# Kernel tuning notes

Measured on AMD Instinct MI355X. Metric: run time of the kernel, lower is better.

## Reference

```python
import jax, jax.numpy as jnp
import numpy as np

IN_EPS = 1e-3   # torch InstanceNorm2d eps in this module
BN_EPS = 1e-5   # torch BatchNorm2d default eps
KNN_K = 6


def instance_norm(x):
    # x: (B, C, N, 1); normalize per (batch, channel) over spatial dims (affine=False)
    m = jnp.mean(x, axis=(2, 3), keepdims=True)
    v = jnp.var(x, axis=(2, 3), keepdims=True)
    return (x - m) / jnp.sqrt(v + IN_EPS)


def batch_norm(x, gamma, beta):
    # training-mode BatchNorm2d: batch statistics over (B, H, W), biased var
    m = jnp.mean(x, axis=(0, 2, 3), keepdims=True)
    v = jnp.var(x, axis=(0, 2, 3), keepdims=True)
    xn = (x - m) / jnp.sqrt(v + BN_EPS)
    return xn * gamma[None, :, None, None] + beta[None, :, None, None]


def conv1x1(x, w, b):
    # x: (B, Cin, N, K), w: (Cout, Cin), b: (Cout,)
    return jnp.einsum('bcnk,oc->bonk', x, w) + b[None, :, None, None]


def graph_feature(x, k):
    # x: (B, C, P). KNN in feature space + edge feature [x_i, x_i - x_j].
    B, C, P = x.shape
    sq = jnp.sum(x * x, axis=1)                      # (B, P)
    gram = jnp.einsum('bcn,bcm->bnm', x, x)          # (B, P, P)
    pd = 2.0 * gram - sq[:, :, None] - sq[:, None, :]  # negative squared distance
    idx = jax.lax.top_k(pd, k)[1]                    # (B, P, k) nearest (incl. self)
    xt = jnp.transpose(x, (0, 2, 1))                 # (B, P, C)
    neigh = jnp.take_along_axis(xt, idx.reshape(B, P * k)[:, :, None], axis=1)
    neigh = neigh.reshape(B, P, k, C)
    center = jnp.broadcast_to(xt[:, :, None, :], (B, P, k, C))
    edge = jnp.concatenate([center, center - neigh], axis=3)  # (B, P, k, 2C)
    return jnp.transpose(edge, (0, 3, 1, 2))         # (B, 2C, P, k)


def reference(data, dp_gamma, dp_beta, dp_w, dp_b, du_gamma, du_beta, du_w, du_b,
              dg_w1, dg_b1, dg_g1, dg_bb1, dg_w2, dg_b2, dg_g2, dg_bb2, sc_w, sc_b):
    x = data                                         # (B, C=128, N, 1)
    # ---- diff_pool ----
    h = jax.nn.relu(batch_norm(instance_norm(x), dp_gamma, dp_beta))
    embed = conv1x1(h, dp_w, dp_b)                   # (B, K=256, N, 1)
    S = jax.nn.softmax(embed[..., 0], axis=2)        # softmax over points -> (B, K, N)
    x_down = jnp.einsum('bcn,bkn->bck', x[..., 0], S)  # (B, C, K)
    feats = jnp.transpose(x_down, (0, 2, 1))         # transpose(1,2): (B, K, C)
    # ---- DGCNN_MAX_Block: channels=K=256, points=C=128, k=6 ----
    edge = graph_feature(feats, KNN_K)               # (B, 2K, C, k)
    g = jax.nn.relu(batch_norm(conv1x1(edge, dg_w1, dg_b1), dg_g1, dg_bb1))
    g = jax.nn.relu(batch_norm(conv1x1(g, dg_w2, dg_b2), dg_g2, dg_bb2))
    g = jnp.max(g, axis=3)                           # max over neighbors -> (B, K, C)
    x2 = jnp.transpose(g, (0, 2, 1))                 # (B, C, K)
    # ---- diff_unpool ----
    h2 = jax.nn.relu(batch_norm(instance_norm(x), du_gamma, du_beta))
    embed2 = conv1x1(h2, du_w, du_b)                 # (B, K, N, 1)
    S2 = jax.nn.softmax(embed2[..., 0], axis=1)      # softmax over clusters -> (B, K, N)
    x_up = jnp.einsum('bck,bkn->bcn', x2, S2)[..., None]  # (B, C, N, 1)
    out = jnp.concatenate([x, x_up], axis=1)         # (B, 2C, N, 1)
    return conv1x1(out, sc_w, sc_b)                  # (B, C, N, 1)


def setup_inputs() -> dict:
    B, C, N, K = 16, 128, 8192, 256
    ks = jax.random.split(jax.random.key(0), 8)
    s = 0.05
    return {
        'data': jax.random.normal(ks[0], (B, C, N, 1), dtype=jnp.float32),
        'dp_gamma': jnp.ones((C,), jnp.float32), 'dp_beta': jnp.zeros((C,), jnp.float32),
        'dp_w': jax.random.normal(ks[1], (K, C), dtype=jnp.float32) * s,
        'dp_b': jnp.zeros((K,), jnp.float32),
        'du_gamma': jnp.ones((C,), jnp.float32), 'du_beta': jnp.zeros((C,), jnp.float32),
        'du_w': jax.random.normal(ks[2], (K, C), dtype=jnp.float32) * s,
        'du_b': jnp.zeros((K,), jnp.float32),
        'dg_w1': jax.random.normal(ks[3], (K, 2 * K), dtype=jnp.float32) * s,
        'dg_b1': jnp.zeros((K,), jnp.float32),
        'dg_g1': jnp.ones((K,), jnp.float32), 'dg_bb1': jnp.zeros((K,), jnp.float32),
        'dg_w2': jax.random.normal(ks[4], (K, K), dtype=jnp.float32) * s,
        'dg_b2': jnp.zeros((K,), jnp.float32),
        'dg_g2': jnp.ones((K,), jnp.float32), 'dg_bb2': jnp.zeros((K,), jnp.float32),
        'sc_w': jax.random.normal(ks[5], (C, 2 * C), dtype=jnp.float32) * s,
        'sc_b': jnp.zeros((C,), jnp.float32),
    }
```

## Files before the change

kernel.cpp:

```cpp
#include <hip/hip_runtime.h>

typedef __attribute__((ext_vector_type(4))) float f32x4;
typedef __attribute__((ext_vector_type(8))) short s16x8;
typedef __attribute__((ext_vector_type(8))) unsigned short u16x8;
typedef __attribute__((ext_vector_type(4))) unsigned short u16x4;

namespace {
constexpr int B_ = 16, C_ = 128, N_ = 8192, K_ = 256, P_ = 128, NB_ = 6;
constexpr int NSP = 8;
}

__device__ __forceinline__ float bf2f(unsigned short h) {
  return __uint_as_float(((unsigned int)h) << 16);
}
__device__ __forceinline__ unsigned short f2bf(float f) {
  unsigned int u = __float_as_uint(f);
  return (unsigned short)((u + 0x7fffu + ((u >> 16) & 1u)) >> 16);
}
__device__ __forceinline__ void gload_lds16(const void* gsrc, void* ldsdst) {
  __builtin_amdgcn_global_load_lds(
      (const __attribute__((address_space(1))) void*)gsrc,
      (__attribute__((address_space(3))) void*)ldsdst, 16, 0, 0);
}

__global__ __launch_bounds__(256) void k_prep(const float* __restrict__ x,
                                              unsigned short* __restrict__ xh,
                                              unsigned short* __restrict__ xcn,
                                              float* __restrict__ pstS,
                                              float* __restrict__ pstQ) {
  const int chunk = blockIdx.x, b = blockIdx.y;
  const int n0 = chunk * 64;
  __shared__ float ts[64][132];
  __shared__ float rs_[2][128], rq_[2][128];
  const int tid = threadIdx.x;
  for (int i = 0; i < 8; i++) {
    int q = tid + i * 256;
    int n4 = q & 15, c = q >> 4;
    float4 v = *reinterpret_cast<const float4*>(x + (size_t)(b * C_ + c) * N_ + n0 + 4 * n4);
    ts[4 * n4 + 0][c] = v.x; ts[4 * n4 + 1][c] = v.y;
    ts[4 * n4 + 2][c] = v.z; ts[4 * n4 + 3][c] = v.w;
    u16x4 p; p[0] = f2bf(v.x); p[1] = f2bf(v.y); p[2] = f2bf(v.z); p[3] = f2bf(v.w);
    *reinterpret_cast<u16x4*>(xcn + (size_t)(b * C_ + c) * N_ + n0 + 4 * n4) = p;
  }
  __syncthreads();
  for (int i = 0; i < 4; i++) {
    int q = tid + i * 256;
    int cg = q & 15, nn = q >> 4;
    u16x8 o;
#pragma unroll
    for (int j = 0; j < 8; j++) o[j] = f2bf(ts[nn][8 * cg + j]);
    *reinterpret_cast<u16x8*>(xh + (size_t)(b * N_ + n0 + nn) * C_ + 8 * cg) = o;
  }
  {
    int c = tid & 127, h = tid >> 7;
    float s = 0.f, ss = 0.f;
    for (int nn = h * 32; nn < h * 32 + 32; nn++) { float v = ts[nn][c]; s += v; ss += v * v; }
    rs_[h][c] = s; rq_[h][c] = ss;
  }
  __syncthreads();
  if (tid < 128) {
    pstS[(chunk * 16 + b) * 128 + tid] = rs_[0][tid] + rs_[1][tid];
    pstQ[(chunk * 16 + b) * 128 + tid] = rq_[0][tid] + rq_[1][tid];
  }
}

__global__ __launch_bounds__(256) void k_wconv(const float* __restrict__ dpw,
                                               const float* __restrict__ duw,
                                               const float* __restrict__ scw,
                                               const float* __restrict__ w1,
                                               const float* __restrict__ w2,
                                               unsigned short* __restrict__ dpwh,
                                               unsigned short* __restrict__ duwh,
                                               unsigned short* __restrict__ scah,
                                               unsigned short* __restrict__ scbh,
                                               unsigned short* __restrict__ w1sh,
                                               unsigned short* __restrict__ w1bh,
                                               unsigned short* __restrict__ w2h) {
  int t = blockIdx.x * 256 + threadIdx.x;
  if (t < 65536) {
    int o = t >> 8, k = t & 255;
    float vb = w1[(size_t)o * 512 + 256 + k];
    w1sh[t] = f2bf(w1[(size_t)o * 512 + k] + vb);
    w1bh[t] = f2bf(vb);
    w2h[t] = f2bf(w2[t]);
  }
  if (t < 32768) { dpwh[t] = f2bf(dpw[t]); duwh[t] = f2bf(duw[t]); }
  if (t < 16384) {
    int o = t >> 7, c = t & 127;
    scah[t] = f2bf(scw[o * 256 + c]);
    scbh[t] = f2bf(scw[o * 256 + 128 + c]);
  }
}

__global__ __launch_bounds__(256) void k_instat_fin(const float* __restrict__ pstS,
                                                    const float* __restrict__ pstQ,
                                                    float* __restrict__ m_o,
                                                    float* __restrict__ v_o,
                                                    float* __restrict__ r_o) {
  int e = blockIdx.x * 256 + threadIdx.x;
  int b = e >> 7, c = e & 127;
  float s = 0.f, q = 0.f;
  for (int ch = 0; ch < 128; ch++) {
    s += pstS[(ch * 16 + b) * 128 + c];
    q += pstQ[(ch * 16 + b) * 128 + c];
  }
  float m = s / N_;
  float v = q / N_ - m * m;
  m_o[e] = m; v_o[e] = v; r_o[e] = rsqrtf(v + 1e-3f);
}

__global__ void k_affine(const float* __restrict__ m_in, const float* __restrict__ v_in,
                         const float* __restrict__ r_in,
                         const float* __restrict__ dpg, const float* __restrict__ dpb,
                         const float* __restrict__ dug, const float* __restrict__ dub,
                         float* __restrict__ a_dp, float* __restrict__ d_dp,
                         float* __restrict__ a_du, float* __restrict__ d_du) {
  int c = threadIdx.x;
  float V = 0.f;
  for (int b = 0; b < B_; b++) { float v = v_in[b * C_ + c]; V += v / (v + 1e-3f); }
  V *= (1.f / B_);
  float R = rsqrtf(V + 1e-5f);
  float gdp = dpg[c], bdp = dpb[c], gdu = dug[c], bdu = dub[c];
  for (int b = 0; b < B_; b++) {
    int i = b * C_ + c;
    float r = r_in[i], m = m_in[i];
    float sdp = r * R * gdp;
    a_dp[i] = sdp; d_dp[i] = -m * sdp + bdp;
    float sdu = r * R * gdu;
    a_du[i] = sdu; d_du[i] = -m * sdu + bdu;
  }
}

template <int MODE>
__global__ __launch_bounds__(256) void k_embed_p(const unsigned short* __restrict__ xh,
                                                 const unsigned short* __restrict__ wh,
                                                 const float* __restrict__ bias,
                                                 const float* __restrict__ aff_a,
                                                 const float* __restrict__ aff_d,
                                                 unsigned short* __restrict__ outp,
                                                 float* __restrict__ psum) {
  const int n0 = blockIdx.x * 128, k0 = blockIdx.y * 128, b = blockIdx.z;
  __shared__ __align__(16) unsigned short smem[2 * 128 * 128];
  unsigned short* tA = smem;
  unsigned short* tB = smem + 128 * 128;
  __shared__ float aff_as[128], aff_ds[128], bias_s[128];
  const int tid = threadIdx.x, lane = tid & 63, wid = tid >> 6;
  const int wr = wid >> 1, wc = wid & 1, l15 = lane & 15, l4 = lane >> 4;
  if (tid < 128) {
    aff_as[tid] = aff_a[b * C_ + tid];
    aff_ds[tid] = aff_d[b * C_ + tid];
    bias_s[tid] = bias[k0 + tid];
  }
#pragma unroll
  for (int i = 0; i < 8; i++) {
    int call = wid * 8 + i;
    int row = call * 4 + (lane >> 4);
    int gch = (lane & 15) ^ (row & 7);
    gload_lds16(wh + (size_t)(k0 + row) * C_ + gch * 8, tA + call * 512);
    gload_lds16(xh + (size_t)(b * N_ + n0 + row) * C_ + gch * 8, tB + call * 512);
  }
  __syncthreads();
  f32x4 acc[4][4] = {};
#pragma unroll
  for (int ks = 0; ks < 128; ks += 32) {
    const int ch = (ks >> 3) + l4;
    s16x8 af[4], bfv[4];
#pragma unroll
    for (int m = 0; m < 4; m++) {
      int row = wr * 64 + m * 16 + l15;
      af[m] = *reinterpret_cast<const s16x8*>(tA + row * 128 + ((ch ^ (row & 7)) << 3));
    }
#pragma unroll
    for (int n = 0; n < 4; n++) {
      int row = wc * 64 + n * 16 + l15;
      s16x8 raw = *reinterpret_cast<const s16x8*>(tB + row * 128 + ((ch ^ (row & 7)) << 3));
      s16x8 h;
#pragma unroll
      for (int j = 0; j < 8; j++) {
        int c = ks + 8 * l4 + j;
        h[j] = (short)f2bf(fmaxf(fmaf(aff_as[c], bf2f((unsigned short)raw[j]), aff_ds[c]), 0.f));
      }
      bfv[n] = h;
    }
#pragma unroll
    for (int m = 0; m < 4; m++)
#pragma unroll
      for (int n = 0; n < 4; n++)
        acc[m][n] = __builtin_amdgcn_mfma_f32_16x16x32_bf16(af[m], bfv[n], acc[m][n], 0, 0, 0);
  }
  __syncthreads();
  unsigned short (*e_s)[136] = reinterpret_cast<unsigned short(*)[136]>(smem);
#pragma unroll
  for (int m = 0; m < 4; m++)
#pragma unroll
    for (int n = 0; n < 4; n++) {
      int kl = wr * 64 + m * 16 + 4 * l4;
      int nl = wc * 64 + n * 16 + l15;
#pragma unroll
      for (int r = 0; r < 4; r++) {
        unsigned short v = f2bf(__expf(acc[m][n][r] + bias_s[kl + r]));
        if (MODE == 0) e_s[kl + r][nl] = v;
        else           e_s[nl][kl + r] = v;
      }
    }
  __syncthreads();
  {
    int row = tid >> 1, half = tid & 1;
    float s = 0.f;
    for (int j = 0; j < 64; j++) s += bf2f(e_s[row][half * 64 + j]);
    s += __shfl_xor(s, 1);
    if (half == 0) {
      if (MODE == 0) psum[((size_t)blockIdx.x * 16 + b) * 256 + k0 + row] = s;
      else           psum[((size_t)blockIdx.y * 16 + b) * 8192 + n0 + row] = s;
    }
  }
  if (MODE == 0) {
    for (int i = 0; i < 8; i++) {
      int q = tid + i * 256;
      int cg = q & 15, kk = q >> 4;
      u16x8 v = *reinterpret_cast<const u16x8*>(&e_s[kk][8 * cg]);
      *reinterpret_cast<u16x8*>(outp + (size_t)(b * K_ + k0 + kk) * N_ + n0 + 8 * cg) = v;
    }
  } else {
    for (int i = 0; i < 8; i++) {
      int q = tid + i * 256;
      int kg = q & 15, nn = q >> 4;
      u16x8 v = *reinterpret_cast<const u16x8*>(&e_s[nn][8 * kg]);
      *reinterpret_cast<u16x8*>(outp + (size_t)(b * N_ + n0 + nn) * K_ + k0 + 8 * kg) = v;
    }
  }
}

__global__ __launch_bounds__(256) void k_rowfin(const float* __restrict__ pS,
                                                float* __restrict__ rden) {
  int e = blockIdx.x * 256 + threadIdx.x;
  int b = e >> 8, k = e & 255;
  float s = 0.f;
  for (int nb = 0; nb < 64; nb++) s += pS[((size_t)nb * 16 + b) * 256 + k];
  rden[e] = 1.f / s;
}

__global__ __launch_bounds__(256) void k_xdown_g(const unsigned short* __restrict__ xcn,
                                                 const unsigned short* __restrict__ Pb,
                                                 float* __restrict__ part) {
  const int k0 = blockIdx.x * 128, sp = blockIdx.y, b = blockIdx.z;
  const int nbase = sp * (N_ / NSP);
  __shared__ __align__(16) unsigned short smem[2 * 128 * 128];
  unsigned short* tA = smem;
  unsigned short* tB = smem + 128 * 128;
  const int tid = threadIdx.x, lane = tid & 63, wid = tid >> 6;
  const int wr = wid >> 1, wc = wid & 1, l15 = lane & 15, l4 = lane >> 4;
  f32x4 acc[4][4] = {};
  for (int nc = 0; nc < N_ / NSP; nc += 128) {
    const int n0 = nbase + nc;
#pragma unroll
    for (int i = 0; i < 8; i++) {
      int call = wid * 8 + i;
      int row = call * 4 + (lane >> 4);
      int gch = (lane & 15) ^ (row & 7);
      gload_lds16(xcn + (size_t)(b * C_ + row) * N_ + n0 + gch * 8, tA + call * 512);
      gload_lds16(Pb + (size_t)(b * K_ + k0 + row) * N_ + n0 + gch * 8, tB + call * 512);
    }
    __syncthreads();
#pragma unroll
    for (int ks = 0; ks < 128; ks += 32) {
      const int ch = (ks >> 3) + l4;
      s16x8 af[4], bfv[4];
#pragma unroll
      for (int m = 0; m < 4; m++) {
        int row = wr * 64 + m * 16 + l15;
        af[m] = *reinterpret_cast<const s16x8*>(tA + row * 128 + ((ch ^ (row & 7)) << 3));
      }
#pragma unroll
      for (int n = 0; n < 4; n++) {
        int row = wc * 64 + n * 16 + l15;
        bfv[n] = *reinterpret_cast<const s16x8*>(tB + row * 128 + ((ch ^ (row & 7)) << 3));
      }
#pragma unroll
      for (int m = 0; m < 4; m++)
#pragma unroll
        for (int n = 0; n < 4; n++)
          acc[m][n] = __builtin_amdgcn_mfma_f32_16x16x32_bf16(af[m], bfv[n], acc[m][n], 0, 0, 0);
    }
    __syncthreads();
  }
#pragma unroll
  for (int m = 0; m < 4; m++)
#pragma unroll
    for (int n = 0; n < 4; n++) {
      int c = wr * 64 + m * 16 + 4 * l4;
      int k = k0 + wc * 64 + n * 16 + l15;
#pragma unroll
      for (int r = 0; r < 4; r++)
        part[((size_t)(sp * B_ + b) * C_ + c + r) * K_ + k] = acc[m][n][r];
    }
}

__global__ __launch_bounds__(256) void k_xdown_red(const float* __restrict__ part,
                                                   const float* __restrict__ rden,
                                                   float* __restrict__ xd,
                                                   unsigned short* __restrict__ xdh) {
  int e = blockIdx.x * 256 + threadIdx.x;
  int k = e % K_;
  int b = e / (K_ * C_);
  float s = 0.f;
  for (int sp = 0; sp < NSP; sp++) s += part[(size_t)sp * (B_ * C_ * K_) + e];
  float v = s * rden[b * K_ + k];
  xd[e] = v;
  xdh[e] = f2bf(v);
}

__global__ __launch_bounds__(256) void k_knn(const float* __restrict__ xd,
                                             int* __restrict__ idx) {
  const int p0 = blockIdx.x * 8, b = blockIdx.y;
  __shared__ float A[8][256];
  __shared__ float Bt[32][132];
  __shared__ float pd_s[8][129];
  __shared__ float sq_s[128], sqh[128];
  const int tid = threadIdx.x;
#pragma unroll
  for (int i = 0; i < 2; i++) {
    int t = tid + i * 256;
    int pp = t >> 6, k4 = t & 63;
    float4 v = *reinterpret_cast<const float4*>(xd + (size_t)(b * C_ + p0 + pp) * K_ + 4 * k4);
    *reinterpret_cast<float4*>(&A[pp][4 * k4]) = v;
  }
  const int q = tid & 127, h = tid >> 7;
  float acc[4] = {};
  float sqacc = 0.f;
  for (int k0 = 0; k0 < K_; k0 += 32) {
    for (int i = 0; i < 4; i++) {
      int t = tid + i * 256;
      int qq = t >> 3, k4 = t & 7;
      float4 v = *reinterpret_cast<const float4*>(xd + (size_t)(b * C_ + qq) * K_ + k0 + 4 * k4);
      Bt[4 * k4 + 0][qq] = v.x; Bt[4 * k4 + 1][qq] = v.y;
      Bt[4 * k4 + 2][qq] = v.z; Bt[4 * k4 + 3][qq] = v.w;
    }
    __syncthreads();
    for (int kk = 0; kk < 32; ++kk) {
      float bv = Bt[kk][q];
#pragma unroll
      for (int i = 0; i < 4; ++i) acc[i] = fmaf(A[h * 4 + i][k0 + kk], bv, acc[i]);
    }
    {
      float s = 0.f;
      for (int kk = h * 16; kk < h * 16 + 16; kk++) { float v = Bt[kk][q]; s += v * v; }
      sqacc += s;
    }
    __syncthreads();
  }
  if (h == 1) sqh[q] = sqacc;
#pragma unroll
  for (int i = 0; i < 4; ++i) pd_s[h * 4 + i][q] = acc[i];
  __syncthreads();
  if (tid < 128) sq_s[tid] = sqacc + sqh[tid];
  __syncthreads();
  const int wv = tid >> 6, lane = tid & 63;
  for (int r = 0; r < 2; r++) {
    int p = wv * 2 + r;
    float v0 = 2.f * pd_s[p][lane] - sq_s[lane];
    float v1 = 2.f * pd_s[p][lane + 64] - sq_s[lane + 64];
    int q0 = lane, q1 = lane + 64;
#pragma unroll
    for (int j = 0; j < NB_; j++) {
      float bv; int bq;
      if (v0 > v1 || (v0 == v1 && q0 < q1)) { bv = v0; bq = q0; } else { bv = v1; bq = q1; }
#pragma unroll
      for (int o = 32; o > 0; o >>= 1) {
        float ov = __shfl_xor(bv, o); int oq = __shfl_xor(bq, o);
        if (ov > bv || (ov == bv && oq < bq)) { bv = ov; bq = oq; }
      }
      if (lane == 0) idx[(b * P_ + p0 + p) * NB_ + j] = bq;
      if (q0 == bq) v0 = -3.0e38f;
      if (q1 == bq) v1 = -3.0e38f;
    }
  }
}

__global__ __launch_bounds__(256) void k_uv_mfma(const unsigned short* __restrict__ xdh,
                                                 const unsigned short* __restrict__ w1sh,
                                                 const unsigned short* __restrict__ w1bh,
                                                 float* __restrict__ Ut, float* __restrict__ Vt) {
  const int o0 = blockIdx.x * 128, which = blockIdx.y, b = blockIdx.z;
  __shared__ __align__(16) unsigned char smemraw[128 * 132 * 4];
  unsigned short* tA = (unsigned short*)smemraw;
  unsigned short* tB = tA + 128 * 128;
  const unsigned short* wsel = which ? w1bh : w1sh;
  const int tid = threadIdx.x, lane = tid & 63, wid = tid >> 6;
  const int wr = wid >> 1, wc = wid & 1, l15 = lane & 15, l4 = lane >> 4;
  f32x4 acc[4][4] = {};
  for (int kh = 0; kh < 256; kh += 128) {
#pragma unroll
    for (int i = 0; i < 8; i++) {
      int call = wid * 8 + i;
      int row = call * 4 + (lane >> 4);
      int gch = (lane & 15) ^ (row & 7);
      gload_lds16(wsel + (size_t)(o0 + row) * 256 + kh + gch * 8, tA + call * 512);
      gload_lds16(xdh + (size_t)(b * P_ + row) * 256 + kh + gch * 8, tB + call * 512);
    }
    __syncthreads();
#pragma unroll
    for (int ks = 0; ks < 128; ks += 32) {
      const int ch = (ks >> 3) + l4;
      s16x8 af[4], bfv[4];
#pragma unroll
      for (int m = 0; m < 4; m++) {
        int row = wr * 64 + m * 16 + l15;
        af[m] = *reinterpret_cast<const s16x8*>(tA + row * 128 + ((ch ^ (row & 7)) << 3));
      }
#pragma unroll
      for (int n = 0; n < 4; n++) {
        int row = wc * 64 + n * 16 + l15;
        bfv[n] = *reinterpret_cast<const s16x8*>(tB + row * 128 + ((ch ^ (row & 7)) << 3));
      }
#pragma unroll
      for (int m = 0; m < 4; m++)
#pragma unroll
        for (int n = 0; n < 4; n++)
          acc[m][n] = __builtin_amdgcn_mfma_f32_16x16x32_bf16(af[m], bfv[n], acc[m][n], 0, 0, 0);
    }
    __syncthreads();
  }
  float (*ef)[132] = (float(*)[132])smemraw;
#pragma unroll
  for (int m = 0; m < 4; m++)
#pragma unroll
    for (int n = 0; n < 4; n++) {
      int ol = wr * 64 + m * 16 + 4 * l4;
      int pl = wc * 64 + n * 16 + l15;
#pragma unroll
      for (int r = 0; r < 4; r++) ef[pl][ol + r] = acc[m][n][r];
    }
  __syncthreads();
  float* outp = which ? Vt : Ut;
  for (int i = 0; i < 16; i++) {
    int q = tid + i * 256;
    int pl = q >> 5, c4 = q & 31;
    float4 v = *reinterpret_cast<const float4*>(&ef[pl][c4 * 4]);
    *reinterpret_cast<float4*>(outp + (size_t)(b * P_ + pl) * 256 + o0 + c4 * 4) = v;
  }
}

__global__ __launch_bounds__(256) void k_edge_t(const float* __restrict__ Ut,
                                                const float* __restrict__ Vt,
                                                const int* __restrict__ idx,
                                                const float* __restrict__ b1,
                                                unsigned short* __restrict__ g1h) {
  __shared__ float b1s[256];
  const int tid = threadIdx.x;
  b1s[tid] = b1[tid];
  __syncthreads();
  const int row0 = blockIdx.x * 16;
  for (int r = 0; r < 16; r++) {
    int row = row0 + r;
    int b = row / 768, pj = row % 768, p = pj / 6;
    int q = idx[(b * P_ + p) * NB_ + (pj % 6)];
    float v = Ut[(size_t)(b * P_ + p) * 256 + tid] + b1s[tid]
            - Vt[(size_t)(b * P_ + q) * 256 + tid];
    g1h[(size_t)row * 256 + tid] = f2bf(v);
  }
}

__global__ __launch_bounds__(256) void k_bnstat_t(const unsigned short* __restrict__ gt,
                                                  float* __restrict__ partS,
                                                  float* __restrict__ partQ) {
  const int tid = threadIdx.x;
  const size_t row0 = (size_t)blockIdx.x * 256;
  float s = 0.f, ss = 0.f;
  for (int r = 0; r < 256; r++) {
    float v = bf2f(gt[(row0 + r) * 256 + tid]);
    s += v; ss += v * v;
  }
  partS[blockIdx.x * 256 + tid] = s;
  partQ[blockIdx.x * 256 + tid] = ss;
}

__global__ __launch_bounds__(256) void k_conv2_mfma(const unsigned short* __restrict__ g1h,
                                                    const unsigned short* __restrict__ w2h,
                                                    const float* __restrict__ b2,
                                                    const float* __restrict__ partS,
                                                    const float* __restrict__ partQ,
                                                    const float* __restrict__ gamma,
                                                    const float* __restrict__ beta,
                                                    unsigned short* __restrict__ g2h) {
  const int n0 = blockIdx.x * 128, o0 = blockIdx.y * 128, b = blockIdx.z;
  __shared__ __align__(16) unsigned short smem[2 * 128 * 128];
  unsigned short* tA = smem;
  unsigned short* tB = smem + 128 * 128;
  __shared__ float scs[256], shs[256], b2s[128];
  const int tid = threadIdx.x, lane = tid & 63, wid = tid >> 6;
  const int wr = wid >> 1, wc = wid & 1, l15 = lane & 15, l4 = lane >> 4;
  {
    float s = 0.f, q = 0.f;
    for (int i = 0; i < 48; i++) { s += partS[i * 256 + tid]; q += partQ[i * 256 + tid]; }
    const float cnt = (float)(B_ * P_ * NB_);
    float m = s / cnt, var = q / cnt - m * m;
    float scale = gamma[tid] * rsqrtf(var + 1e-5f);
    scs[tid] = scale; shs[tid] = -m * scale + beta[tid];
  }
  if (tid < 128) b2s[tid] = b2[o0 + tid];
  f32x4 acc[4][4] = {};
  for (int kh = 0; kh < 256; kh += 128) {
#pragma unroll
    for (int i = 0; i < 8; i++) {
      int call = wid * 8 + i;
      int row = call * 4 + (lane >> 4);
      int gch = (lane & 15) ^ (row & 7);
      gload_lds16(w2h + (size_t)(o0 + row) * 256 + kh + gch * 8, tA + call * 512);
      gload_lds16(g1h + (size_t)(b * 768 + n0 + row) * 256 + kh + gch * 8, tB + call * 512);
    }
    __syncthreads();
#pragma unroll
    for (int ks = 0; ks < 128; ks += 32) {
      const int ch = (ks >> 3) + l4;
      s16x8 af[4], bfv[4];
#pragma unroll
      for (int m = 0; m < 4; m++) {
        int row = wr * 64 + m * 16 + l15;
        af[m] = *reinterpret_cast<const s16x8*>(tA + row * 128 + ((ch ^ (row & 7)) << 3));
      }
#pragma unroll
      for (int n = 0; n < 4; n++) {
        int row = wc * 64 + n * 16 + l15;
        s16x8 raw = *reinterpret_cast<const s16x8*>(tB + row * 128 + ((ch ^ (row & 7)) << 3));
        s16x8 h;
#pragma unroll
        for (int j = 0; j < 8; j++) {
          int c = kh + ks + 8 * l4 + j;
          h[j] = (short)f2bf(fmaxf(fmaf(scs[c], bf2f((unsigned short)raw[j]), shs[c]), 0.f));
        }
        bfv[n] = h;
      }
#pragma unroll
      for (int m = 0; m < 4; m++)
#pragma unroll
        for (int n = 0; n < 4; n++)
          acc[m][n] = __builtin_amdgcn_mfma_f32_16x16x32_bf16(af[m], bfv[n], acc[m][n], 0, 0, 0);
    }
    __syncthreads();
  }
  unsigned short (*e_s)[136] = reinterpret_cast<unsigned short(*)[136]>(smem);
#pragma unroll
  for (int m = 0; m < 4; m++)
#pragma unroll
    for (int n = 0; n < 4; n++) {
      int ol = wr * 64 + m * 16 + 4 * l4;
      int nl = wc * 64 + n * 16 + l15;
#pragma unroll
      for (int r = 0; r < 4; r++)
        e_s[nl][ol + r] = f2bf(acc[m][n][r] + b2s[ol + r]);
    }
  __syncthreads();
  for (int i = 0; i < 8; i++) {
    int q = tid + i * 256;
    int og = q & 15, nl = q >> 4;
    u16x8 v = *reinterpret_cast<const u16x8*>(&e_s[nl][8 * og]);
    *reinterpret_cast<u16x8*>(g2h + (size_t)(b * 768 + n0 + nl) * 256 + o0 + 8 * og) = v;
  }
}

__global__ __launch_bounds__(256) void k_gmax_t(const unsigned short* __restrict__ g2h,
                                                const float* __restrict__ partS,
                                                const float* __restrict__ partQ,
                                                const float* __restrict__ gamma,
                                                const float* __restrict__ beta,
                                                unsigned short* __restrict__ gmaxh) {
  const int o0 = blockIdx.x * 128, b = blockIdx.y;
  __shared__ float scS[128], shS[128];
  const int tid = threadIdx.x;
  if (tid < 128) {
    int o = o0 + tid;
    float s = 0.f, q = 0.f;
    for (int i = 0; i < 48; i++) { s += partS[i * 256 + o]; q += partQ[i * 256 + o]; }
    const float cnt = (float)(B_ * P_ * NB_);
    float m = s / cnt, var = q / cnt - m * m;
    float scale = gamma[o] * rsqrtf(var + 1e-5f);
    scS[tid] = scale; shS[tid] = -m * scale + beta[o];
  }
  __syncthreads();
  const int ol = tid & 127, ph = tid >> 7;
  const int o = o0 + ol;
  const float sc = scS[ol], sh = shS[ol];
  for (int p8 = ph * 64; p8 < ph * 64 + 64; p8 += 8) {
    u16x8 pack;
#pragma unroll
    for (int pi = 0; pi < 8; pi++) {
      int p = p8 + pi;
      float m = 0.f;
#pragma unroll
      for (int j = 0; j < NB_; j++) {
        float v = bf2f(g2h[(size_t)(b * 768 + p * 6 + j) * 256 + o]);
        m = fmaxf(m, fmaf(sc, v, sh));
      }
      pack[pi] = f2bf(m);
    }
    *reinterpret_cast<u16x8*>(gmaxh + (size_t)(b * 256 + o) * P_ + p8) = pack;
  }
}

__global__ __launch_bounds__(256) void k_m2_mfma(const unsigned short* __restrict__ gmaxh,
                                                 const unsigned short* __restrict__ scbh,
                                                 unsigned short* __restrict__ M2h) {
  const int k0 = blockIdx.x * 128, b = blockIdx.y;
  __shared__ __align__(16) unsigned short smem[2 * 128 * 128];
  unsigned short* tA = smem;
  unsigned short* tB = smem + 128 * 128;
  const int tid = threadIdx.x, lane = tid & 63, wid = tid >> 6;
  const int wr = wid >> 1, wc = wid & 1, l15 = lane & 15, l4 = lane >> 4;
#pragma unroll
  for (int i = 0; i < 8; i++) {
    int call = wid * 8 + i;
    int row = call * 4 + (lane >> 4);
    int gch = (lane & 15) ^ (row & 7);
    gload_lds16(scbh + (size_t)row * P_ + gch * 8, tA + call * 512);
    gload_lds16(gmaxh + (size_t)(b * 256 + k0 + row) * P_ + gch * 8, tB + call * 512);
  }
  __syncthreads();
  f32x4 acc[4][4] = {};
#pragma unroll
  for (int ks = 0; ks < 128; ks += 32) {
    const int ch = (ks >> 3) + l4;
    s16x8 af[4], bfv[4];
#pragma unroll
    for (int m = 0; m < 4; m++) {
      int row = wr * 64 + m * 16 + l15;
      af[m] = *reinterpret_cast<const s16x8*>(tA + row * 128 + ((ch ^ (row & 7)) << 3));
    }
#pragma unroll
    for (int n = 0; n < 4; n++) {
      int row = wc * 64 + n * 16 + l15;
      bfv[n] = *reinterpret_cast<const s16x8*>(tB + row * 128 + ((ch ^ (row & 7)) << 3));
    }
#pragma unroll
    for (int m = 0; m < 4; m++)
#pragma unroll
      for (int n = 0; n < 4; n++)
        acc[m][n] = __builtin_amdgcn_mfma_f32_16x16x32_bf16(af[m], bfv[n], acc[m][n], 0, 0, 0);
  }
  __syncthreads();
  unsigned short (*e_s)[136] = reinterpret_cast<unsigned short(*)[136]>(smem);
#pragma unroll
  for (int m = 0; m < 4; m++)
#pragma unroll
    for (int n = 0; n < 4; n++) {
      int ol = wr * 64 + m * 16 + 4 * l4;
      int kl = wc * 64 + n * 16 + l15;
#pragma unroll
      for (int r = 0; r < 4; r++)
        e_s[ol + r][kl] = f2bf(acc[m][n][r]);
    }
  __syncthreads();
  for (int i = 0; i < 8; i++) {
    int q = tid + i * 256;
    int kg = q & 15, oo = q >> 4;
    u16x8 v = *reinterpret_cast<const u16x8*>(&e_s[oo][8 * kg]);
    *reinterpret_cast<u16x8*>(M2h + (size_t)(b * C_ + oo) * K_ + k0 + 8 * kg) = v;
  }
}

__global__ __launch_bounds__(256) void k_final_g(const unsigned short* __restrict__ PT,
                                                 const unsigned short* __restrict__ xh,
                                                 const unsigned short* __restrict__ M2h,
                                                 const unsigned short* __restrict__ scah,
                                                 const float* __restrict__ scb,
                                                 const float* __restrict__ pC,
                                                 float* __restrict__ out) {
  const int n0 = blockIdx.x * 128, b = blockIdx.y;
  __shared__ __align__(16) unsigned short smem[2 * 128 * 128];
  unsigned short* tA = smem;
  unsigned short* tB = smem + 128 * 128;
  __shared__ float rs2s[128], scb_s[128];
  const int tid = threadIdx.x, lane = tid & 63, wid = tid >> 6;
  const int wr = wid >> 1, wc = wid & 1, l15 = lane & 15, l4 = lane >> 4;
  if (tid < 128) {
    float d = pC[(size_t)b * 8192 + n0 + tid] + pC[(size_t)(16 + b) * 8192 + n0 + tid];
    rs2s[tid] = 1.f / d;
    scb_s[tid] = scb[tid];
  }
  f32x4 acc[4][4] = {};
  for (int kh = 0; kh < K_; kh += 128) {
#pragma unroll
    for (int i = 0; i < 8; i++) {
      int call = wid * 8 + i;
      int row = call * 4 + (lane >> 4);
      int gch = (lane & 15) ^ (row & 7);
      gload_lds16(M2h + (size_t)(b * C_ + row) * K_ + kh + gch * 8, tA + call * 512);
      gload_lds16(PT + (size_t)(b * N_ + n0 + row) * K_ + kh + gch * 8, tB + call * 512);
    }
    __syncthreads();
#pragma unroll
    for (int ks = 0; ks < 128; ks += 32) {
      const int ch = (ks >> 3) + l4;
      s16x8 af[4], bfv[4];
#pragma unroll
      for (int m = 0; m < 4; m++) {
        int row = wr * 64 + m * 16 + l15;
        af[m] = *reinterpret_cast<const s16x8*>(tA + row * 128 + ((ch ^ (row & 7)) << 3));
      }
#pragma unroll
      for (int n = 0; n < 4; n++) {
        int row = wc * 64 + n * 16 + l15;
        bfv[n] = *reinterpret_cast<const s16x8*>(tB + row * 128 + ((ch ^ (row & 7)) << 3));
      }
#pragma unroll
      for (int m = 0; m < 4; m++)
#pragma unroll
        for (int n = 0; n < 4; n++)
          acc[m][n] = __builtin_amdgcn_mfma_f32_16x16x32_bf16(af[m], bfv[n], acc[m][n], 0, 0, 0);
    }
    __syncthreads();
  }
#pragma unroll
  for (int n = 0; n < 4; n++) {
    float rv = rs2s[wc * 64 + n * 16 + l15];
#pragma unroll
    for (int m = 0; m < 4; m++) {
      acc[m][n][0] *= rv; acc[m][n][1] *= rv; acc[m][n][2] *= rv; acc[m][n][3] *= rv;
    }
  }
#pragma unroll
  for (int i = 0; i < 8; i++) {
    int call = wid * 8 + i;
    int row = call * 4 + (lane >> 4);
    int gch = (lane & 15) ^ (row & 7);
    gload_lds16(scah + (size_t)row * C_ + gch * 8, tA + call * 512);
    gload_lds16(xh + (size_t)(b * N_ + n0 + row) * C_ + gch * 8, tB + call * 512);
  }
  __syncthreads();
#pragma unroll
  for (int ks = 0; ks < 128; ks += 32) {
    const int ch = (ks >> 3) + l4;
    s16x8 af[4], bfv[4];
#pragma unroll
    for (int m = 0; m < 4; m++) {
      int row = wr * 64 + m * 16 + l15;
      af[m] = *reinterpret_cast<const s16x8*>(tA + row * 128 + ((ch ^ (row & 7)) << 3));
    }
#pragma unroll
    for (int n = 0; n < 4; n++) {
      int row = wc * 64 + n * 16 + l15;
      bfv[n] = *reinterpret_cast<const s16x8*>(tB + row * 128 + ((ch ^ (row & 7)) << 3));
    }
#pragma unroll
    for (int m = 0; m < 4; m++)
#pragma unroll
      for (int n = 0; n < 4; n++)
        acc[m][n] = __builtin_amdgcn_mfma_f32_16x16x32_bf16(af[m], bfv[n], acc[m][n], 0, 0, 0);
  }
#pragma unroll
  for (int m = 0; m < 4; m++)
#pragma unroll
    for (int n = 0; n < 4; n++) {
      int o = wr * 64 + m * 16 + 4 * l4;
      int nn = n0 + wc * 64 + n * 16 + l15;
#pragma unroll
      for (int r = 0; r < 4; r++)
        out[(size_t)(b * C_ + o + r) * N_ + nn] = acc[m][n][r] + scb_s[o + r];
    }
}

extern "C" void kernel_launch(void* const* d_in, const int* in_sizes, int n_in,
                              void* d_out, int out_size, void* d_ws, size_t ws_size,
                              hipStream_t stream) {
  (void)in_sizes; (void)n_in; (void)out_size; (void)ws_size;
  const float* x      = (const float*)d_in[0];
  const float* dpg    = (const float*)d_in[1];
  const float* dpb    = (const float*)d_in[2];
  const float* dpw    = (const float*)d_in[3];
  const float* dpbias = (const float*)d_in[4];
  const float* dug    = (const float*)d_in[5];
  const float* dub    = (const float*)d_in[6];
  const float* duw    = (const float*)d_in[7];
  const float* dubias = (const float*)d_in[8];
  const float* w1     = (const float*)d_in[9];
  const float* b1     = (const float*)d_in[10];
  const float* g1g    = (const float*)d_in[11];
  const float* g1b    = (const float*)d_in[12];
  const float* w2     = (const float*)d_in[13];
  const float* b2     = (const float*)d_in[14];
  const float* g2g    = (const float*)d_in[15];
  const float* g2b    = (const float*)d_in[16];
  const float* scw    = (const float*)d_in[17];
  const float* scb    = (const float*)d_in[18];
  float* out = (float*)d_out;
  float* ws  = (float*)d_ws;

  unsigned short* EB  = (unsigned short*)ws;
  unsigned short* xh  = (unsigned short*)(ws + 16777216);
  unsigned short* xcn = (unsigned short*)(ws + 25165824);
  float* base  = ws + 33554432;
  float* m_in  = base;
  float* v_in  = m_in + 2048;
  float* r_in  = v_in + 2048;
  float* a_dp  = r_in + 2048;
  float* d_dp  = a_dp + 2048;
  float* a_du  = d_dp + 2048;
  float* d_du  = a_du + 2048;
  float* rden  = d_du + 2048;
  float* xd    = rden + 4096;
  float* Ut    = xd + 524288;
  float* Vt    = Ut + 524288;
  int*   idxb  = (int*)(Vt + 524288);
  float* partS = (float*)(idxb + 12288);
  float* partQ = partS + 12288;
  float* pstS  = partQ + 12288;
  float* pstQ  = pstS + 262144;
  float* pS    = pstQ + 262144;
  float* pC    = pS + 262144;
  unsigned short* xdh  = (unsigned short*)(pC + 262144);
  unsigned short* dpwh = xdh + 524288;
  unsigned short* duwh = dpwh + 32768;
  unsigned short* scah = duwh + 32768;
  unsigned short* scbh = scah + 16384;
  unsigned short* w1sh = scbh + 16384;
  unsigned short* w1bh = w1sh + 65536;
  unsigned short* w2h  = w1bh + 65536;
  unsigned short* M2h  = w2h + 65536;
  float* part = (float*)(M2h + 524288);
  unsigned short* g1h   = (unsigned short*)part;
  unsigned short* g2h   = g1h + 3145728;
  unsigned short* gmaxh = g2h + 3145728;

  k_prep<<<dim3(128, 16), 256, 0, stream>>>(x, xh, xcn, pstS, pstQ);
  k_wconv<<<dim3(256), 256, 0, stream>>>(dpw, duw, scw, w1, w2,
                                         dpwh, duwh, scah, scbh, w1sh, w1bh, w2h);
  k_instat_fin<<<dim3(8), 256, 0, stream>>>(pstS, pstQ, m_in, v_in, r_in);
  k_affine<<<1, 128, 0, stream>>>(m_in, v_in, r_in, dpg, dpb, dug, dub, a_dp, d_dp, a_du, d_du);
  k_embed_p<0><<<dim3(64, 2, 16), 256, 0, stream>>>(xh, dpwh, dpbias, a_dp, d_dp, EB, pS);
  k_rowfin<<<dim3(16), 256, 0, stream>>>(pS, rden);
  k_xdown_g<<<dim3(2, NSP, 16), 256, 0, stream>>>(xcn, EB, part);
  k_xdown_red<<<dim3(2048), 256, 0, stream>>>(part, rden, xd, xdh);
  k_knn<<<dim3(16, 16), 256, 0, stream>>>(xd, idxb);
  k_uv_mfma<<<dim3(2, 2, 16), 256, 0, stream>>>(xdh, w1sh, w1bh, Ut, Vt);
  k_edge_t<<<dim3(768), 256, 0, stream>>>(Ut, Vt, idxb, b1, g1h);
  k_bnstat_t<<<dim3(48), 256, 0, stream>>>(g1h, partS, partQ);
  k_conv2_mfma<<<dim3(6, 2, 16), 256, 0, stream>>>(g1h, w2h, b2, partS, partQ, g1g, g1b, g2h);
  k_bnstat_t<<<dim3(48), 256, 0, stream>>>(g2h, partS, partQ);
  k_gmax_t<<<dim3(2, 16), 256, 0, stream>>>(g2h, partS, partQ, g2g, g2b, gmaxh);
  k_m2_mfma<<<dim3(2, 16), 256, 0, stream>>>(gmaxh, scbh, M2h);
  k_embed_p<1><<<dim3(64, 2, 16), 256, 0, stream>>>(xh, duwh, dubias, a_du, d_du, EB, pC);
  k_final_g<<<dim3(64, 16), 256, 0, stream>>>(EB, xh, M2h, scah, scb, pC, out);
}
```

Before: 256.4 us.

## Fuse softmax-embed GEMMs into xdown and final GEMMs, dropping EB buffer

The diff-pool embedding (affine+ReLU, 1x1 conv, exp) is now computed per 128-point chunk inside the x_down GEMM kernel, with row sums accumulated in-kernel. Likewise the diff-unpool embedding is recomputed inside the final output kernel, and column sums are kept in shared memory. This removes the large bf16 intermediate EB and its global write/read round trips, plus two launches. In exchange the pool kernel runs its embed GEMM on a small grid with large LDS use, reducing parallelism and occupancy.

```diff
diff --git a/kernel.cpp b/kernel.cpp
--- a/kernel.cpp
+++ b/kernel.cpp
@@ -131,104 +131,130 @@
   }
 }
 
-template <int MODE>
-__global__ __launch_bounds__(256) void k_embed_p(const unsigned short* __restrict__ xh,
-                                                 const unsigned short* __restrict__ wh,
-                                                 const float* __restrict__ bias,
-                                                 const float* __restrict__ aff_a,
-                                                 const float* __restrict__ aff_d,
-                                                 unsigned short* __restrict__ outp,
-                                                 float* __restrict__ psum) {
-  const int n0 = blockIdx.x * 128, k0 = blockIdx.y * 128, b = blockIdx.z;
-  __shared__ __align__(16) unsigned short smem[2 * 128 * 128];
-  unsigned short* tA = smem;
-  unsigned short* tB = smem + 128 * 128;
+__global__ __launch_bounds__(256) void k_dp_fused(const unsigned short* __restrict__ xh,
+                                                  const unsigned short* __restrict__ xcn,
+                                                  const unsigned short* __restrict__ dpwh,
+                                                  const float* __restrict__ dpbias,
+                                                  const float* __restrict__ a_dp,
+                                                  const float* __restrict__ d_dp,
+                                                  float* __restrict__ part,
+                                                  float* __restrict__ pS) {
+  const int kt = blockIdx.x, sp = blockIdx.y, b = blockIdx.z;
+  const int k0 = kt * 128;
+  const int nbase = sp * (N_ / NSP);
+  __shared__ __align__(16) unsigned short bufW[128 * 128];
+  __shared__ __align__(16) unsigned short bufX[128 * 128];
+  __shared__ __align__(16) unsigned short bufC[128 * 128];
+  __shared__ __align__(16) unsigned short bufP[128 * 128];
   __shared__ float aff_as[128], aff_ds[128], bias_s[128];
   const int tid = threadIdx.x, lane = tid & 63, wid = tid >> 6;
   const int wr = wid >> 1, wc = wid & 1, l15 = lane & 15, l4 = lane >> 4;
   if (tid < 128) {
-    aff_as[tid] = aff_a[b * C_ + tid];
-    aff_ds[tid] = aff_d[b * C_ + tid];
-    bias_s[tid] = bias[k0 + tid];
+    aff_as[tid] = a_dp[b * C_ + tid];
+    aff_ds[tid] = d_dp[b * C_ + tid];
+    bias_s[tid] = dpbias[k0 + tid];
   }
 #pragma unroll
   for (int i = 0; i < 8; i++) {
     int call = wid * 8 + i;
     int row = call * 4 + (lane >> 4);
     int gch = (lane & 15) ^ (row & 7);
-    gload_lds16(wh + (size_t)(k0 + row) * C_ + gch * 8, tA + call * 512);
-    gload_lds16(xh + (size_t)(b * N_ + n0 + row) * C_ + gch * 8, tB + call * 512);
-  }
-  __syncthreads();
-  f32x4 acc[4][4] = {};
-#pragma unroll
-  for (int ks = 0; ks < 128; ks += 32) {
-    const int ch = (ks >> 3) + l4;
-    s16x8 af[4], bfv[4];
-#pragma unroll
-    for (int m = 0; m < 4; m++) {
-      int row = wr * 64 + m * 16 + l15;
-      af[m] = *reinterpret_cast<const s16x8*>(tA + row * 128 + ((ch ^ (row & 7)) << 3));
-    }
+    gload_lds16(dpwh + (size_t)(k0 + row) * C_ + gch * 8, bufW + call * 512);
+  }
+  f32x4 acc2[4][4] = {};
+  const int prow = tid >> 1, phalf = tid & 1;
+  float rowsum = 0.f;
+  for (int nc = 0; nc < N_ / NSP; nc += 128) {
+    const int n0 = nbase + nc;
+#pragma unroll
+    for (int i = 0; i < 8; i++) {
+      int call = wid * 8 + i;
+      int row = call * 4 + (lane >> 4);
+      int gch = (lane & 15) ^ (row & 7);
+      gload_lds16(xh + (size_t)(b * N_ + n0 + row) * C_ + gch * 8, bufX + call * 512);
+      gload_lds16(xcn + (size_t)(b * C_ + row) * N_ + n0 + gch * 8, bufC + call * 512);
+    }
+    __syncthreads();
+    f32x4 acc1[4][4] = {};
+#pragma unroll
+    for (int ks = 0; ks < 128; ks += 32) {
+      const int ch = (ks >> 3) + l4;
+      s16x8 af[4], bfv[4];
+#pragma unroll
+      for (int m = 0; m < 4; m++) {
+        int row = wr * 64 + m * 16 + l15;
+        af[m] = *reinterpret_cast<const s16x8*>(bufW + row * 128 + ((ch ^ (row & 7)) << 3));
+      }
+#pragma unroll
+      for (int n = 0; n < 4; n++) {
+        int row = wc * 64 + n * 16 + l15;
+        s16x8 raw = *reinterpret_cast<const s16x8*>(bufX + row * 128 + ((ch ^ (row & 7)) << 3));
+        s16x8 h;
+#pragma unroll
+        for (int j = 0; j < 8; j++) {
+          int c = ks + 8 * l4 + j;
+          h[j] = (short)f2bf(fmaxf(fmaf(aff_as[c], bf2f((unsigned short)raw[j]), aff_ds[c]), 0.f));
+        }
+        bfv[n] = h;
+      }
+#pragma unroll
+      for (int m = 0; m < 4; m++)
+#pragma unroll
+        for (int n = 0; n < 4; n++)
+          acc1[m][n] = __builtin_amdgcn_mfma_f32_16x16x32_bf16(af[m], bfv[n], acc1[m][n], 0, 0, 0);
+    }
+#pragma unroll
+    for (int m = 0; m < 4; m++)
+#pragma unroll
+      for (int n = 0; n < 4; n++) {
+        int kl = wr * 64 + m * 16 + 4 * l4;
+        int nl = wc * 64 + n * 16 + l15;
+#pragma unroll
+        for (int r = 0; r < 4; r++) {
+          unsigned short v = f2bf(__expf(acc1[m][n][r] + bias_s[kl + r]));
+          bufP[(kl + r) * 128 + ((((nl >> 3) ^ ((kl + r) & 7)) << 3) | (nl & 7))] = v;
+        }
+      }
+    __syncthreads();
+    {
+      float s = 0.f;
+      for (int j = 0; j < 64; j++) s += bf2f(bufP[prow * 128 + phalf * 64 + j]);
+      rowsum += s;
+    }
+#pragma unroll
+    for (int ks = 0; ks < 128; ks += 32) {
+      const int ch = (ks >> 3) + l4;
+      s16x8 af[4], bfv[4];
+#pragma unroll
+      for (int m = 0; m < 4; m++) {
+        int row = wr * 64 + m * 16 + l15;
+        af[m] = *reinterpret_cast<const s16x8*>(bufC + row * 128 + ((ch ^ (row & 7)) << 3));
+      }
+#pragma unroll
+      for (int n = 0; n < 4; n++) {
+        int row = wc * 64 + n * 16 + l15;
+        bfv[n] = *reinterpret_cast<const s16x8*>(bufP + row * 128 + ((ch ^ (row & 7)) << 3));
+      }
+#pragma unroll
+      for (int m = 0; m < 4; m++)
+#pragma unroll
+        for (int n = 0; n < 4; n++)
+          acc2[m][n] = __builtin_amdgcn_mfma_f32_16x16x32_bf16(af[m], bfv[n], acc2[m][n], 0, 0, 0);
+    }
+    __syncthreads();
+  }
+#pragma unroll
+  for (int m = 0; m < 4; m++)
 #pragma unroll
     for (int n = 0; n < 4; n++) {
-      int row = wc * 64 + n * 16 + l15;
-      s16x8 raw = *reinterpret_cast<const s16x8*>(tB + row * 128 + ((ch ^ (row & 7)) << 3));
-      s16x8 h;
-#pragma unroll
-      for (int j = 0; j < 8; j++) {
-        int c = ks + 8 * l4 + j;
-        h[j] = (short)f2bf(fmaxf(fmaf(aff_as[c], bf2f((unsigned short)raw[j]), aff_ds[c]), 0.f));
-      }
-      bfv[n] = h;
-    }
-#pragma unroll
-    for (int m = 0; m < 4; m++)
-#pragma unroll
-      for (int n = 0; n < 4; n++)
-        acc[m][n] = __builtin_amdgcn_mfma_f32_16x16x32_bf16(af[m], bfv[n], acc[m][n], 0, 0, 0);
-  }
-  __syncthreads();
-  unsigned short (*e_s)[136] = reinterpret_cast<unsigned short(*)[136]>(smem);
-#pragma unroll
-  for (int m = 0; m < 4; m++)
-#pragma unroll
-    for (int n = 0; n < 4; n++) {
-      int kl = wr * 64 + m * 16 + 4 * l4;
-      int nl = wc * 64 + n * 16 + l15;
-#pragma unroll
-      for (int r = 0; r < 4; r++) {
-        unsigned short v = f2bf(__expf(acc[m][n][r] + bias_s[kl + r]));
-        if (MODE == 0) e_s[kl + r][nl] = v;
-        else           e_s[nl][kl + r] = v;
-      }
-    }
-  __syncthreads();
-  {
-    int row = tid >> 1, half = tid & 1;
-    float s = 0.f;
-    for (int j = 0; j < 64; j++) s += bf2f(e_s[row][half * 64 + j]);
-    s += __shfl_xor(s, 1);
-    if (half == 0) {
-      if (MODE == 0) psum[((size_t)blockIdx.x * 16 + b) * 256 + k0 + row] = s;
-      else           psum[((size_t)blockIdx.y * 16 + b) * 8192 + n0 + row] = s;
-    }
-  }
-  if (MODE == 0) {
-    for (int i = 0; i < 8; i++) {
-      int q = tid + i * 256;
-      int cg = q & 15, kk = q >> 4;
-      u16x8 v = *reinterpret_cast<const u16x8*>(&e_s[kk][8 * cg]);
-      *reinterpret_cast<u16x8*>(outp + (size_t)(b * K_ + k0 + kk) * N_ + n0 + 8 * cg) = v;
-    }
-  } else {
-    for (int i = 0; i < 8; i++) {
-      int q = tid + i * 256;
-      int kg = q & 15, nn = q >> 4;
-      u16x8 v = *reinterpret_cast<const u16x8*>(&e_s[nn][8 * kg]);
-      *reinterpret_cast<u16x8*>(outp + (size_t)(b * N_ + n0 + nn) * K_ + k0 + 8 * kg) = v;
-    }
-  }
+      int c = wr * 64 + m * 16 + 4 * l4;
+      int k = k0 + wc * 64 + n * 16 + l15;
+#pragma unroll
+      for (int r = 0; r < 4; r++)
+        part[((size_t)(sp * B_ + b) * C_ + c + r) * K_ + k] = acc2[m][n][r];
+    }
+  rowsum += __shfl_xor(rowsum, 1);
+  if (phalf == 0) pS[((size_t)sp * 16 + b) * 256 + k0 + prow] = rowsum;
 }
 
 __global__ __launch_bounds__(256) void k_rowfin(const float* __restrict__ pS,
@@ -236,64 +262,8 @@
   int e = blockIdx.x * 256 + threadIdx.x;
   int b = e >> 8, k = e & 255;
   float s = 0.f;
-  for (int nb = 0; nb < 64; nb++) s += pS[((size_t)nb * 16 + b) * 256 + k];
+  for (int sp = 0; sp < NSP; sp++) s += pS[((size_t)sp * 16 + b) * 256 + k];
   rden[e] = 1.f / s;
-}
-
-__global__ __launch_bounds__(256) void k_xdown_g(const unsigned short* __restrict__ xcn,
-                                                 const unsigned short* __restrict__ Pb,
-                                                 float* __restrict__ part) {
-  const int k0 = blockIdx.x * 128, sp = blockIdx.y, b = blockIdx.z;
-  const int nbase = sp * (N_ / NSP);
-  __shared__ __align__(16) unsigned short smem[2 * 128 * 128];
-  unsigned short* tA = smem;
-  unsigned short* tB = smem + 128 * 128;
-  const int tid = threadIdx.x, lane = tid & 63, wid = tid >> 6;
-  const int wr = wid >> 1, wc = wid & 1, l15 = lane & 15, l4 = lane >> 4;
-  f32x4 acc[4][4] = {};
-  for (int nc = 0; nc < N_ / NSP; nc += 128) {
-    const int n0 = nbase + nc;
-#pragma unroll
-    for (int i = 0; i < 8; i++) {
-      int call = wid * 8 + i;
-      int row = call * 4 + (lane >> 4);
-      int gch = (lane & 15) ^ (row & 7);
-      gload_lds16(xcn + (size_t)(b * C_ + row) * N_ + n0 + gch * 8, tA + call * 512);
-      gload_lds16(Pb + (size_t)(b * K_ + k0 + row) * N_ + n0 + gch * 8, tB + call * 512);
-    }
-    __syncthreads();
-#pragma unroll
-    for (int ks = 0; ks < 128; ks += 32) {
-      const int ch = (ks >> 3) + l4;
-      s16x8 af[4], bfv[4];
-#pragma unroll
-      for (int m = 0; m < 4; m++) {
-        int row = wr * 64 + m * 16 + l15;
-        af[m] = *reinterpret_cast<const s16x8*>(tA + row * 128 + ((ch ^ (row & 7)) << 3));
-      }
-#pragma unroll
-      for (int n = 0; n < 4; n++) {
-        int row = wc * 64 + n * 16 + l15;
-        bfv[n] = *reinterpret_cast<const s16x8*>(tB + row * 128 + ((ch ^ (row & 7)) << 3));
-      }
-#pragma unroll
-      for (int m = 0; m < 4; m++)
-#pragma unroll
-        for (int n = 0; n < 4; n++)
-          acc[m][n] = __builtin_amdgcn_mfma_f32_16x16x32_bf16(af[m], bfv[n], acc[m][n], 0, 0, 0);
-    }
-    __syncthreads();
-  }
-#pragma unroll
-  for (int m = 0; m < 4; m++)
-#pragma unroll
-    for (int n = 0; n < 4; n++) {
-      int c = wr * 64 + m * 16 + 4 * l4;
-      int k = k0 + wc * 64 + n * 16 + l15;
-#pragma unroll
-      for (int r = 0; r < 4; r++)
-        part[((size_t)(sp * B_ + b) * C_ + c + r) * K_ + k] = acc[m][n][r];
-    }
 }
 
 __global__ __launch_bounds__(256) void k_xdown_red(const float* __restrict__ part,
@@ -658,36 +628,48 @@
   }
 }
 
-__global__ __launch_bounds__(256) void k_final_g(const unsigned short* __restrict__ PT,
-                                                 const unsigned short* __restrict__ xh,
+__global__ __launch_bounds__(256) void k_final_f(const unsigned short* __restrict__ xh,
+                                                 const unsigned short* __restrict__ duwh,
+                                                 const float* __restrict__ dubias,
+                                                 const float* __restrict__ a_du,
+                                                 const float* __restrict__ d_du,
                                                  const unsigned short* __restrict__ M2h,
                                                  const unsigned short* __restrict__ scah,
                                                  const float* __restrict__ scb,
-                                                 const float* __restrict__ pC,
                                                  float* __restrict__ out) {
   const int n0 = blockIdx.x * 128, b = blockIdx.y;
-  __shared__ __align__(16) unsigned short smem[2 * 128 * 128];
-  unsigned short* tA = smem;
-  unsigned short* tB = smem + 128 * 128;
-  __shared__ float rs2s[128], scb_s[128];
+  __shared__ __align__(16) unsigned short bufX[128 * 128];
+  __shared__ __align__(16) unsigned short bufA[128 * 128];
+  __shared__ __align__(16) unsigned short bufP[128 * 128];
+  __shared__ float aff_as[128], aff_ds[128], scb_s[128], psum_s[128], bias_s[128];
   const int tid = threadIdx.x, lane = tid & 63, wid = tid >> 6;
   const int wr = wid >> 1, wc = wid & 1, l15 = lane & 15, l4 = lane >> 4;
   if (tid < 128) {
-    float d = pC[(size_t)b * 8192 + n0 + tid] + pC[(size_t)(16 + b) * 8192 + n0 + tid];
-    rs2s[tid] = 1.f / d;
+    aff_as[tid] = a_du[b * C_ + tid];
+    aff_ds[tid] = d_du[b * C_ + tid];
     scb_s[tid] = scb[tid];
+    psum_s[tid] = 0.f;
+  }
+#pragma unroll
+  for (int i = 0; i < 8; i++) {
+    int call = wid * 8 + i;
+    int row = call * 4 + (lane >> 4);
+    int gch = (lane & 15) ^ (row & 7);
+    gload_lds16(xh + (size_t)(b * N_ + n0 + row) * C_ + gch * 8, bufX + call * 512);
   }
   f32x4 acc[4][4] = {};
+  const int prow = tid >> 1, phalf = tid & 1;
   for (int kh = 0; kh < K_; kh += 128) {
+    if (tid < 128) bias_s[tid] = dubias[kh + tid];
 #pragma unroll
     for (int i = 0; i < 8; i++) {
       int call = wid * 8 + i;
       int row = call * 4 + (lane >> 4);
       int gch = (lane & 15) ^ (row & 7);
-      gload_lds16(M2h + (size_t)(b * C_ + row) * K_ + kh + gch * 8, tA + call * 512);
-      gload_lds16(PT + (size_t)(b * N_ + n0 + row) * K_ + kh + gch * 8, tB + call * 512);
-    }
-    __syncthreads();
+      gload_lds16(duwh + (size_t)(kh + row) * C_ + gch * 8, bufA + call * 512);
+    }
+    __syncthreads();
+    f32x4 acc1[4][4] = {};
 #pragma unroll
     for (int ks = 0; ks < 128; ks += 32) {
       const int ch = (ks >> 3) + l4;
@@ -695,12 +677,66 @@
 #pragma unroll
       for (int m = 0; m < 4; m++) {
         int row = wr * 64 + m * 16 + l15;
-        af[m] = *reinterpret_cast<const s16x8*>(tA + row * 128 + ((ch ^ (row & 7)) << 3));
+        af[m] = *reinterpret_cast<const s16x8*>(bufA + row * 128 + ((ch ^ (row & 7)) << 3));
       }
 #pragma unroll
       for (int n = 0; n < 4; n++) {
         int row = wc * 64 + n * 16 + l15;
-        bfv[n] = *reinterpret_cast<const s16x8*>(tB + row * 128 + ((ch ^ (row & 7)) << 3));
+        s16x8 raw = *reinterpret_cast<const s16x8*>(bufX + row * 128 + ((ch ^ (row & 7)) << 3));
+        s16x8 h;
+#pragma unroll
+        for (int j = 0; j < 8; j++) {
+          int c = ks + 8 * l4 + j;
+          h[j] = (short)f2bf(fmaxf(fmaf(aff_as[c], bf2f((unsigned short)raw[j]), aff_ds[c]), 0.f));
+        }
+        bfv[n] = h;
+      }
+#pragma unroll
+      for (int m = 0; m < 4; m++)
+#pragma unroll
+        for (int n = 0; n < 4; n++)
+          acc1[m][n] = __builtin_amdgcn_mfma_f32_16x16x32_bf16(af[m], bfv[n], acc1[m][n], 0, 0, 0);
+    }
+    __syncthreads();
+#pragma unroll
+    for (int m = 0; m < 4; m++)
+#pragma unroll
+      for (int n = 0; n < 4; n++) {
+        int kl = wr * 64 + m * 16 + 4 * l4;
+        int nl = wc * 64 + n * 16 + l15;
+#pragma unroll
+        for (int r = 0; r < 4; r++) {
+          unsigned short v = f2bf(__expf(acc1[m][n][r] + bias_s[kl + r]));
+          bufP[nl * 128 + (((((kl + r) >> 3) ^ (nl & 7)) << 3) | ((kl + r) & 7))] = v;
+        }
+      }
+#pragma unroll
+    for (int i = 0; i < 8; i++) {
+      int call = wid * 8 + i;
+      int row = call * 4 + (lane >> 4);
+      int gch = (lane & 15) ^ (row & 7);
+      gload_lds16(M2h + (size_t)(b * C_ + row) * K_ + kh + gch * 8, bufA + call * 512);
+    }
+    __syncthreads();
+    {
+      float s = 0.f;
+      for (int j = 0; j < 64; j++) s += bf2f(bufP[prow * 128 + phalf * 64 + j]);
+      s += __shfl_xor(s, 1);
+      if (phalf == 0) psum_s[prow] += s;
+    }
+#pragma unroll
+    for (int ks = 0; ks < 128; ks += 32) {
+      const int ch = (ks >> 3) + l4;
+      s16x8 af[4], bfv[4];
+#pragma unroll
+      for (int m = 0; m < 4; m++) {
+        int row = wr * 64 + m * 16 + l15;
+        af[m] = *reinterpret_cast<const s16x8*>(bufA + row * 128 + ((ch ^ (row & 7)) << 3));
+      }
+#pragma unroll
+      for (int n = 0; n < 4; n++) {
+        int row = wc * 64 + n * 16 + l15;
+        bfv[n] = *reinterpret_cast<const s16x8*>(bufP + row * 128 + ((ch ^ (row & 7)) << 3));
       }
 #pragma unroll
       for (int m = 0; m < 4; m++)
@@ -712,7 +748,7 @@
   }
 #pragma unroll
   for (int n = 0; n < 4; n++) {
-    float rv = rs2s[wc * 64 + n * 16 + l15];
+    float rv = 1.f / psum_s[wc * 64 + n * 16 + l15];
 #pragma unroll
     for (int m = 0; m < 4; m++) {
       acc[m][n][0] *= rv; acc[m][n][1] *= rv; acc[m][n][2] *= rv; acc[m][n][3] *= rv;
@@ -723,8 +759,7 @@
     int call = wid * 8 + i;
     int row = call * 4 + (lane >> 4);
     int gch = (lane & 15) ^ (row & 7);
-    gload_lds16(scah + (size_t)row * C_ + gch * 8, tA + call * 512);
-    gload_lds16(xh + (size_t)(b * N_ + n0 + row) * C_ + gch * 8, tB + call * 512);
+    gload_lds16(scah + (size_t)row * C_ + gch * 8, bufA + call * 512);
   }
   __syncthreads();
 #pragma unroll
@@ -734,12 +769,12 @@
 #pragma unroll
     for (int m = 0; m < 4; m++) {
       int row = wr * 64 + m * 16 + l15;
-      af[m] = *reinterpret_cast<const s16x8*>(tA + row * 128 + ((ch ^ (row & 7)) << 3));
+      af[m] = *reinterpret_cast<const s16x8*>(bufA + row * 128 + ((ch ^ (row & 7)) << 3));
     }
 #pragma unroll
     for (int n = 0; n < 4; n++) {
       int row = wc * 64 + n * 16 + l15;
-      bfv[n] = *reinterpret_cast<const s16x8*>(tB + row * 128 + ((ch ^ (row & 7)) << 3));
+      bfv[n] = *reinterpret_cast<const s16x8*>(bufX + row * 128 + ((ch ^ (row & 7)) << 3));
     }
 #pragma unroll
     for (int m = 0; m < 4; m++)
@@ -785,7 +820,6 @@
   float* out = (float*)d_out;
   float* ws  = (float*)d_ws;
 
-  unsigned short* EB  = (unsigned short*)ws;
   unsigned short* xh  = (unsigned short*)(ws + 16777216);
   unsigned short* xcn = (unsigned short*)(ws + 25165824);
   float* base  = ws + 33554432;
@@ -806,8 +840,7 @@
   float* pstS  = partQ + 12288;
   float* pstQ  = pstS + 262144;
   float* pS    = pstQ + 262144;
-  float* pC    = pS + 262144;
-  unsigned short* xdh  = (unsigned short*)(pC + 262144);
+  unsigned short* xdh  = (unsigned short*)(pS + 262144);
   unsigned short* dpwh = xdh + 524288;
   unsigned short* duwh = dpwh + 32768;
   unsigned short* scah = duwh + 32768;
@@ -826,9 +859,8 @@
                                          dpwh, duwh, scah, scbh, w1sh, w1bh, w2h);
   k_instat_fin<<<dim3(8), 256, 0, stream>>>(pstS, pstQ, m_in, v_in, r_in);
   k_affine<<<1, 128, 0, stream>>>(m_in, v_in, r_in, dpg, dpb, dug, dub, a_dp, d_dp, a_du, d_du);
-  k_embed_p<0><<<dim3(64, 2, 16), 256, 0, stream>>>(xh, dpwh, dpbias, a_dp, d_dp, EB, pS);
+  k_dp_fused<<<dim3(2, NSP, 16), 256, 0, stream>>>(xh, xcn, dpwh, dpbias, a_dp, d_dp, part, pS);
   k_rowfin<<<dim3(16), 256, 0, stream>>>(pS, rden);
-  k_xdown_g<<<dim3(2, NSP, 16), 256, 0, stream>>>(xcn, EB, part);
   k_xdown_red<<<dim3(2048), 256, 0, stream>>>(part, rden, xd, xdh);
   k_knn<<<dim3(16, 16), 256, 0, stream>>>(xd, idxb);
   k_uv_mfma<<<dim3(2, 2, 16), 256, 0, stream>>>(xdh, w1sh, w1bh, Ut, Vt);
@@ -838,6 +870,5 @@
   k_bnstat_t<<<dim3(48), 256, 0, stream>>>(g2h, partS, partQ);
   k_gmax_t<<<dim3(2, 16), 256, 0, stream>>>(g2h, partS, partQ, g2g, g2b, gmaxh);
   k_m2_mfma<<<dim3(2, 16), 256, 0, stream>>>(gmaxh, scbh, M2h);
-  k_embed_p<1><<<dim3(64, 2, 16), 256, 0, stream>>>(xh, duwh, dubias, a_du, d_du, EB, pC);
-  k_final_g<<<dim3(64, 16), 256, 0, stream>>>(EB, xh, M2h, scah, scb, pC, out);
-}
+  k_final_f<<<dim3(64, 16), 256, 0, stream>>>(xh, duwh, dubias, a_du, d_du, M2h, scah, scb, out);
+}
```

Result: no change. 252.7 us (-1.5%).
